# Optimization experiments

Hardware: AMD Instinct MI355X
Metric: run time of the kernel (lower is better)

## Reference

```python
import jax, jax.numpy as jnp
import numpy as np

T, V, D, L, H, F, R = 1024, 17, 1024, 2, 16, 4096, 32
DH = D // H
LORA_SCALE = 2.0  # lora_alpha / r = 64 / 32
MASK_ID = 16
NEG = jnp.float32(-1e9)


def setup_inputs() -> dict:
    key = jax.random.key(0)
    ks = iter(jax.random.split(key, 64))
    def p(shape, std):
        return jax.random.normal(next(ks), shape, jnp.float32) * std
    inp = {
        "packed_context": jax.random.randint(next(ks), (T,), 0, V),
        "cu_seq_lens": jnp.sort(jax.random.randint(next(ks), (5,), 0, T)),
        "max_seq_len": T,
        "row_coords": jax.random.randint(next(ks), (T,), 0, 64),
        "col_coords": jax.random.randint(next(ks), (T,), 0, 64),
        "num_diffusion_steps": 2,
        "E": p((V, D), 0.02),  # embed rows actually used: weight[:vocab_size]
    }
    shapes = {"q": (D, D), "k": (D, D), "v": (D, D), "o": (D, D),
              "g": (D, F), "u": (D, F), "d": (F, D)}
    for nm, (di, do) in shapes.items():
        inp["W" + nm] = p((L, di, do), di ** -0.5)  # frozen NF4 base weight (dequantized)
        inp["A" + nm] = p((L, di, R), di ** -0.5)   # LoRA A
        inp["B" + nm] = p((L, R, do), 0.01)          # LoRA B (nonzero for grad testing)
    inp["ln1"] = jnp.ones((L, D), jnp.float32)
    inp["ln2"] = jnp.ones((L, D), jnp.float32)
    inp["lnf"] = jnp.ones((D,), jnp.float32)
    return inp


def _rms(x, w):
    return x * jax.lax.rsqrt(jnp.mean(x * x, axis=-1, keepdims=True) + 1e-6) * w


def _lora(x, W, A, B):
    # fused base matmul + low-rank LoRA delta
    return x @ W + LORA_SCALE * ((x @ A) @ B)


def _denoise_step(soft, E, Wq, Aq, Bq, Wk, Ak, Bk, Wv, Av, Bv, Wo, Ao, Bo,
                  Wg, Ag, Bg, Wu, Au, Bu, Wd, Ad, Bd, ln1, ln2, lnf, causal_bias):
    # soft-token embedding: [T,V] @ [V,D]
    x = soft @ E
    inv_sqrt_dh = jnp.float32(1.0 / np.sqrt(DH))
    for l in range(L):
        h = _rms(x, ln1[l])
        q = _lora(h, Wq[l], Aq[l], Bq[l]).reshape(T, H, DH)
        k = _lora(h, Wk[l], Ak[l], Bk[l]).reshape(T, H, DH)
        v = _lora(h, Wv[l], Av[l], Bv[l]).reshape(T, H, DH)
        scores = jnp.einsum('qhd,khd->hqk', q, k) * inv_sqrt_dh + causal_bias
        att = jax.nn.softmax(scores, axis=-1)
        ctx = jnp.einsum('hqk,khd->qhd', att, v).reshape(T, D)
        x = x + _lora(ctx, Wo[l], Ao[l], Bo[l])
        h2 = _rms(x, ln2[l])
        ff = jax.nn.silu(_lora(h2, Wg[l], Ag[l], Bg[l])) * _lora(h2, Wu[l], Au[l], Bu[l])
        x = x + _lora(ff, Wd[l], Ad[l], Bd[l])
    logits = _rms(x, lnf) @ E.T  # tied head over the 17-token task vocab
    return jax.nn.softmax(logits, axis=-1)


def reference(packed_context, cu_seq_lens, max_seq_len, row_coords, col_coords,
              num_diffusion_steps, E, Wq, Aq, Bq, Wk, Ak, Bk, Wv, Av, Bv,
              Wo, Ao, Bo, Wg, Ag, Bg, Wu, Au, Bu, Wd, Ad, Bd, ln1, ln2, lnf):
    causal_bias = jnp.where(jnp.tril(jnp.ones((T, T), bool)), jnp.float32(0.0), NEG)
    is_prompt = (packed_context != MASK_ID)[:, None]  # [T,1]
    ctx_onehot = jax.nn.one_hot(packed_context, V, dtype=jnp.float32)
    soft = jnp.zeros((T, V), jnp.float32).at[:, MASK_ID].set(1.0)
    for _ in range(int(num_diffusion_steps)):
        refined = _denoise_step(soft, E, Wq, Aq, Bq, Wk, Ak, Bk, Wv, Av, Bv,
                                Wo, Ao, Bo, Wg, Ag, Bg, Wu, Au, Bu, Wd, Ad, Bd,
                                ln1, ln2, lnf, causal_bias)
        soft = jnp.where(is_prompt, ctx_onehot, refined)
    return jnp.argmax(soft, axis=-1)
```

## Files before the change

### kernel.cpp

```cpp
#include <hip/hip_runtime.h>
#include <hip/hip_bf16.h>

#define T_LEN 1024
#define D_DIM 1024
#define V_DIM 17
#define H_NUM 16
#define DH_DIM 64
#define F_DIM 4096
#define R_LORA 32
#define N_LAYERS 2
#define N_STEPS 2
#define MASK_ID 16
#define LORA_SCALE 2.0f

typedef __attribute__((ext_vector_type(8))) short bfx8;
typedef __attribute__((ext_vector_type(4))) float f32x4;

typedef unsigned short ushort_t;
typedef unsigned int uint_t;

#define AS1 __attribute__((address_space(1)))
#define AS3 __attribute__((address_space(3)))

__device__ __forceinline__ void gload16(const ushort_t* g, ushort_t* l) {
    __builtin_amdgcn_global_load_lds((const AS1 void*)(const void*)g,
                                     (AS3 void*)(void*)l, 16, 0, 0);
}

__device__ __forceinline__ ushort_t f2bf(float v) {
    __hip_bfloat16 h = __float2bfloat16(v);
    return __builtin_bit_cast(unsigned short, h);
}
__device__ __forceinline__ float bf2f(ushort_t u) {
    return __uint_as_float(((uint_t)u) << 16);
}
__device__ __forceinline__ void split4_store(float y0, float y1, float y2, float y3,
                                             ushort_t* __restrict__ hi, ushort_t* __restrict__ lo,
                                             size_t idx) {
    ushort_t h0 = f2bf(y0), h1 = f2bf(y1), h2 = f2bf(y2), h3 = f2bf(y3);
    ushort_t l0 = f2bf(y0 - bf2f(h0));
    ushort_t l1 = f2bf(y1 - bf2f(h1));
    ushort_t l2 = f2bf(y2 - bf2f(h2));
    ushort_t l3 = f2bf(y3 - bf2f(h3));
    uint2 hv, lv;
    hv.x = (uint_t)h0 | ((uint_t)h1 << 16);
    hv.y = (uint_t)h2 | ((uint_t)h3 << 16);
    lv.x = (uint_t)l0 | ((uint_t)l1 << 16);
    lv.y = (uint_t)l2 | ((uint_t)l3 << 16);
    *(uint2*)(hi + idx) = hv;
    *(uint2*)(lo + idx) = lv;
}

__global__ void init_soft_kernel(float* __restrict__ soft) {
    int idx = blockIdx.x * blockDim.x + threadIdx.x;
    if (idx < T_LEN * V_DIM) {
        soft[idx] = ((idx % V_DIM) == MASK_ID) ? 1.0f : 0.0f;
    }
}

__global__ __launch_bounds__(256) void embed_kernel(const float* __restrict__ soft,
                                                    const float* __restrict__ E,
                                                    float* __restrict__ x) {
    int t = blockIdx.x;
    __shared__ float srow[V_DIM];
    if (threadIdx.x < V_DIM) srow[threadIdx.x] = soft[t * V_DIM + threadIdx.x];
    __syncthreads();
    for (int d = threadIdx.x; d < D_DIM; d += 256) {
        float acc = 0.f;
        #pragma unroll
        for (int v = 0; v < V_DIM; v++) acc += srow[v] * E[v * D_DIM + d];
        x[(size_t)t * D_DIM + d] = acc;
    }
}

__global__ __launch_bounds__(256) void fold_kernel(
    const float* __restrict__ W,
    const float* __restrict__ A,
    const float* __restrict__ Bm,
    ushort_t* __restrict__ oHi,
    ushort_t* __restrict__ oLo,
    int K, int N)
{
    const int l = blockIdx.z;
    W   += (size_t)l * K * N;
    A   += (size_t)l * K * R_LORA;
    Bm  += (size_t)l * R_LORA * N;
    oHi += (size_t)l * K * N;
    oLo += (size_t)l * K * N;
    __shared__ uint_t tile[64][65];
    const int tid = threadIdx.x;
    const int n0 = blockIdx.x * 64, k0 = blockIdx.y * 64;
    {
        const int nl = tid & 63, kq = tid >> 6;
        float breg[R_LORA];
        #pragma unroll
        for (int r = 0; r < R_LORA; r++) breg[r] = Bm[(size_t)r * N + n0 + nl];
        for (int i = 0; i < 16; i++) {
            const int kl = kq * 16 + i;
            const size_t kgl = (size_t)(k0 + kl);
            const float4* arow4 = (const float4*)(A + kgl * R_LORA);
            float acc = 0.f;
            #pragma unroll
            for (int r4 = 0; r4 < 8; r4++) {
                float4 a = arow4[r4];
                acc = fmaf(a.x, breg[r4 * 4 + 0], acc);
                acc = fmaf(a.y, breg[r4 * 4 + 1], acc);
                acc = fmaf(a.z, breg[r4 * 4 + 2], acc);
                acc = fmaf(a.w, breg[r4 * 4 + 3], acc);
            }
            float val = W[kgl * N + n0 + nl] + LORA_SCALE * acc;
            ushort_t h = f2bf(val);
            ushort_t l2 = f2bf(val - bf2f(h));
            tile[kl][nl] = ((uint_t)h << 16) | (uint_t)l2;
        }
    }
    __syncthreads();
    {
        const int nl = tid >> 2;
        const int kc0 = (tid & 3) * 16;
        ushort_t hb[16], lb[16];
        #pragma unroll
        for (int i = 0; i < 16; i++) {
            uint_t pk = tile[kc0 + i][nl];
            hb[i] = (ushort_t)(pk >> 16);
            lb[i] = (ushort_t)(pk & 0xffffu);
        }
        size_t idx = (size_t)(n0 + nl) * K + k0 + kc0;
        *(uint4*)(oHi + idx)     = *(uint4*)&hb[0];
        *(uint4*)(oHi + idx + 8) = *(uint4*)&hb[8];
        *(uint4*)(oLo + idx)     = *(uint4*)&lb[0];
        *(uint4*)(oLo + idx + 8) = *(uint4*)&lb[8];
    }
}

__global__ __launch_bounds__(256) void rms_split_kernel(
    const float* __restrict__ x, const float* __restrict__ w,
    ushort_t* __restrict__ hi, ushort_t* __restrict__ lo)
{
    const int t = blockIdx.x, tid = threadIdx.x;
    const float* xr = x + (size_t)t * D_DIM;
    float4 xv = *(const float4*)(xr + tid * 4);
    float ss = xv.x * xv.x + xv.y * xv.y + xv.z * xv.z + xv.w * xv.w;
    __shared__ float red[4];
    const int lane = tid & 63, wv = tid >> 6;
    #pragma unroll
    for (int off = 32; off > 0; off >>= 1) ss += __shfl_xor(ss, off);
    if (lane == 0) red[wv] = ss;
    __syncthreads();
    ss = red[0] + red[1] + red[2] + red[3];
    const float r = 1.0f / sqrtf(ss * (1.0f / D_DIM) + 1e-6f);
    const float4 wv4 = *(const float4*)(w + tid * 4);
    size_t base = (size_t)t * D_DIM + tid * 4;
    split4_store(xv.x * r * wv4.x, xv.y * r * wv4.y, xv.z * r * wv4.z, xv.w * r * wv4.w,
                 hi, lo, base);
}

__global__ __launch_bounds__(256) void add4_rms_split_kernel(
    float* __restrict__ x, const float* __restrict__ p0, const float* __restrict__ p1,
    const float* __restrict__ p2, const float* __restrict__ p3,
    const float* __restrict__ w, ushort_t* __restrict__ hi, ushort_t* __restrict__ lo)
{
    const int t = blockIdx.x, tid = threadIdx.x;
    size_t base = (size_t)t * D_DIM + tid * 4;
    float4 xv = *(const float4*)(x + base);
    float4 a = *(const float4*)(p0 + base);
    float4 b = *(const float4*)(p1 + base);
    float4 c = *(const float4*)(p2 + base);
    float4 d = *(const float4*)(p3 + base);
    xv.x += a.x + b.x + c.x + d.x;
    xv.y += a.y + b.y + c.y + d.y;
    xv.z += a.z + b.z + c.z + d.z;
    xv.w += a.w + b.w + c.w + d.w;
    *(float4*)(x + base) = xv;
    float ss = xv.x * xv.x + xv.y * xv.y + xv.z * xv.z + xv.w * xv.w;
    __shared__ float red[4];
    const int lane = tid & 63, wv = tid >> 6;
    #pragma unroll
    for (int off = 32; off > 0; off >>= 1) ss += __shfl_xor(ss, off);
    if (lane == 0) red[wv] = ss;
    __syncthreads();
    ss = red[0] + red[1] + red[2] + red[3];
    const float r = 1.0f / sqrtf(ss * (1.0f / D_DIM) + 1e-6f);
    const float4 wv4 = *(const float4*)(w + tid * 4);
    split4_store(xv.x * r * wv4.x, xv.y * r * wv4.y, xv.z * r * wv4.z, xv.w * r * wv4.w,
                 hi, lo, base);
}

struct GemmJob {
    const ushort_t* Bh;
    const ushort_t* Bl;
    float* Cf;
    ushort_t* Ch;
    ushort_t* Cl;
    int k0, k1;
};

__global__ __launch_bounds__(256) void gemm128_kernel(
    const ushort_t* __restrict__ Ahi, const ushort_t* __restrict__ Alo,
    int K, int N, GemmJob j0, GemmJob j1, GemmJob j2, GemmJob j3)
{
    GemmJob jb = (blockIdx.z == 0) ? j0 : (blockIdx.z == 1) ? j1 : (blockIdx.z == 2) ? j2 : j3;
    __shared__ ushort_t Ash[128][32];
    __shared__ ushort_t Asl[128][32];
    __shared__ ushort_t Bsh[128][32];
    __shared__ ushort_t Bsl[128][32];

    const int tid = threadIdx.x, lane = tid & 63, w = tid >> 6;
    const int l15 = lane & 15, lg = lane >> 4;
    const int m0 = blockIdx.y * 128, n0 = blockIdx.x * 128;
    const int wm = (w >> 1) * 64, wn = (w & 1) * 64;

    const int r0 = w * 32;
    const int rsub = lane >> 2;
    const int cs = lane & 3;
    const int csl = (cs ^ ((rsub >> 1) & 3)) * 8;
    const int rsl = (lg ^ ((l15 >> 1) & 3)) * 8;

    f32x4 acc[4][4];
    #pragma unroll
    for (int i = 0; i < 4; i++)
        #pragma unroll
        for (int j = 0; j < 4; j++) acc[i][j] = f32x4{0.f, 0.f, 0.f, 0.f};

    const size_t rowA = (size_t)(m0 + r0 + rsub) * K;
    const size_t rowB = (size_t)(n0 + r0 + rsub) * K;
    const size_t rstep = (size_t)16 * K;

    for (int kk = jb.k0; kk < jb.k1; kk += 32) {
        {
            const ushort_t* a0 = Ahi + rowA + kk + csl;
            const ushort_t* a1 = Alo + rowA + kk + csl;
            const ushort_t* b0 = jb.Bh + rowB + kk + csl;
            const ushort_t* b1 = jb.Bl + rowB + kk + csl;
            gload16(a0,         &Ash[r0][0]);
            gload16(a0 + rstep, &Ash[r0 + 16][0]);
            gload16(a1,         &Asl[r0][0]);
            gload16(a1 + rstep, &Asl[r0 + 16][0]);
            gload16(b0,         &Bsh[r0][0]);
            gload16(b0 + rstep, &Bsh[r0 + 16][0]);
            gload16(b1,         &Bsl[r0][0]);
            gload16(b1 + rstep, &Bsl[r0 + 16][0]);
        }
        __syncthreads();
        bfx8 bh[4], bl[4];
        #pragma unroll
        for (int ni = 0; ni < 4; ni++) {
            bh[ni] = *(const bfx8*)&Bsh[wn + ni * 16 + l15][rsl];
            bl[ni] = *(const bfx8*)&Bsl[wn + ni * 16 + l15][rsl];
        }
        #pragma unroll
        for (int mi = 0; mi < 4; mi++) {
            bfx8 ah = *(const bfx8*)&Ash[wm + mi * 16 + l15][rsl];
            bfx8 al = *(const bfx8*)&Asl[wm + mi * 16 + l15][rsl];
            #pragma unroll
            for (int ni = 0; ni < 4; ni++) {
                acc[mi][ni] = __builtin_amdgcn_mfma_f32_16x16x32_bf16(ah, bh[ni], acc[mi][ni], 0, 0, 0);
                acc[mi][ni] = __builtin_amdgcn_mfma_f32_16x16x32_bf16(ah, bl[ni], acc[mi][ni], 0, 0, 0);
                acc[mi][ni] = __builtin_amdgcn_mfma_f32_16x16x32_bf16(al, bh[ni], acc[mi][ni], 0, 0, 0);
            }
        }
        __syncthreads();
    }

    if (jb.Cf) {
        #pragma unroll
        for (int mi = 0; mi < 4; mi++)
            #pragma unroll
            for (int ni = 0; ni < 4; ni++) {
                int col = n0 + wn + ni * 16 + l15;
                #pragma unroll
                for (int i = 0; i < 4; i++) {
                    int row = m0 + wm + mi * 16 + lg * 4 + i;
                    jb.Cf[(size_t)row * N + col] = acc[mi][ni][i];
                }
            }
    } else {
        #pragma unroll
        for (int mi = 0; mi < 4; mi++)
            #pragma unroll
            for (int ni = 0; ni < 4; ni++) {
                int col = n0 + wn + ni * 16 + l15;
                #pragma unroll
                for (int i = 0; i < 4; i++) {
                    int row = m0 + wm + mi * 16 + lg * 4 + i;
                    size_t idx = (size_t)row * N + col;
                    float v = acc[mi][ni][i];
                    ushort_t h = f2bf(v);
                    jb.Ch[idx] = h;
                    jb.Cl[idx] = f2bf(v - bf2f(h));
                }
            }
    }
}

__global__ void add4_kernel(float* __restrict__ x, const float* __restrict__ p0,
                            const float* __restrict__ p1, const float* __restrict__ p2,
                            const float* __restrict__ p3, int n4) {
    int i = blockIdx.x * blockDim.x + threadIdx.x;
    if (i < n4) {
        float4 xv = *(const float4*)(x + (size_t)i * 4);
        float4 a = *(const float4*)(p0 + (size_t)i * 4);
        float4 b = *(const float4*)(p1 + (size_t)i * 4);
        float4 c = *(const float4*)(p2 + (size_t)i * 4);
        float4 d = *(const float4*)(p3 + (size_t)i * 4);
        xv.x += a.x + b.x + c.x + d.x;
        xv.y += a.y + b.y + c.y + d.y;
        xv.z += a.z + b.z + c.z + d.z;
        xv.w += a.w + b.w + c.w + d.w;
        *(float4*)(x + (size_t)i * 4) = xv;
    }
}

#define KS_PAD 72
#define P_PAD 72
__global__ __launch_bounds__(256, 1) void attn_mfma_kernel(
    const ushort_t* __restrict__ qh, const ushort_t* __restrict__ ql,
    const ushort_t* __restrict__ kh, const ushort_t* __restrict__ kl,
    const ushort_t* __restrict__ vh, const ushort_t* __restrict__ vl,
    ushort_t* __restrict__ chi, ushort_t* __restrict__ clo)
{
    __shared__ ushort_t Ksh[64][KS_PAD];
    __shared__ ushort_t Ksl[64][KS_PAD];
    __shared__ ushort_t VTh[64][KS_PAD];
    __shared__ ushort_t VTl[64][KS_PAD];
    __shared__ ushort_t Ph[4][16][P_PAD];
    __shared__ ushort_t Pl[4][16][P_PAD];

    const int qt = blockIdx.x, hh = blockIdx.y;
    const int tid = threadIdx.x, w = tid >> 6, lane = tid & 63;
    const int l15 = lane & 15, lg = lane >> 4;
    const int q0 = qt * 64;
    const int hcol = hh * DH_DIM;

    bfx8 qa_h[2], qa_l[2];
    {
        size_t qrow = (size_t)(q0 + w * 16 + l15) * D_DIM + hcol;
        #pragma unroll
        for (int ks = 0; ks < 2; ks++) {
            qa_h[ks] = *(const bfx8*)(qh + qrow + ks * 32 + lg * 8);
            qa_l[ks] = *(const bfx8*)(ql + qrow + ks * 32 + lg * 8);
        }
    }

    f32x4 o[4];
    #pragma unroll
    for (int ni = 0; ni < 4; ni++) o[ni] = f32x4{0.f, 0.f, 0.f, 0.f};
    float mrun[4], lrun[4];
    #pragma unroll
    for (int i = 0; i < 4; i++) { mrun[i] = -3.0e38f; lrun[i] = 0.f; }

    const int srow = tid >> 2;
    const int sseg = (tid & 3) * 16;
    const int vp = tid & 31;
    const int vd0 = (tid >> 5) * 8;

    for (int kt = 0; kt <= qt; kt++) {
        __syncthreads();
        {
            size_t src = (size_t)(kt * 64 + srow) * D_DIM + hcol + sseg;
            *(uint4*)&Ksh[srow][sseg]     = *(const uint4*)(kh + src);
            *(uint4*)&Ksh[srow][sseg + 8] = *(const uint4*)(kh + src + 8);
            *(uint4*)&Ksl[srow][sseg]     = *(const uint4*)(kl + src);
            *(uint4*)&Ksl[srow][sseg + 8] = *(const uint4*)(kl + src + 8);
        }
        {
            size_t s0 = (size_t)(kt * 64 + 2 * vp) * D_DIM + hcol + vd0;
            uint4 h0 = *(const uint4*)(vh + s0);
            uint4 h1 = *(const uint4*)(vh + s0 + D_DIM);
            uint4 l0 = *(const uint4*)(vl + s0);
            uint4 l1 = *(const uint4*)(vl + s0 + D_DIM);
            const ushort_t* a = (const ushort_t*)&h0;
            const ushort_t* b = (const ushort_t*)&h1;
            const ushort_t* c = (const ushort_t*)&l0;
            const ushort_t* d = (const ushort_t*)&l1;
            #pragma unroll
            for (int j = 0; j < 8; j++) {
                *(uint_t*)&VTh[vd0 + j][2 * vp] = (uint_t)a[j] | ((uint_t)b[j] << 16);
                *(uint_t*)&VTl[vd0 + j][2 * vp] = (uint_t)c[j] | ((uint_t)d[j] << 16);
            }
        }
        __syncthreads();

        f32x4 s[4];
        #pragma unroll
        for (int ni = 0; ni < 4; ni++) s[ni] = f32x4{0.f, 0.f, 0.f, 0.f};
        #pragma unroll
        for (int ks = 0; ks < 2; ks++) {
            #pragma unroll
            for (int ni = 0; ni < 4; ni++) {
                bfx8 bh = *(const bfx8*)&Ksh[ni * 16 + l15][ks * 32 + lg * 8];
                bfx8 bl = *(const bfx8*)&Ksl[ni * 16 + l15][ks * 32 + lg * 8];
                s[ni] = __builtin_amdgcn_mfma_f32_16x16x32_bf16(qa_h[ks], bh, s[ni], 0, 0, 0);
                s[ni] = __builtin_amdgcn_mfma_f32_16x16x32_bf16(qa_h[ks], bl, s[ni], 0, 0, 0);
                s[ni] = __builtin_amdgcn_mfma_f32_16x16x32_bf16(qa_l[ks], bh, s[ni], 0, 0, 0);
            }
        }

        const int kbase = kt * 64;
        float rmax[4];
        #pragma unroll
        for (int i = 0; i < 4; i++) rmax[i] = -3.0e38f;
        #pragma unroll
        for (int ni = 0; ni < 4; ni++) {
            int kc = kbase + ni * 16 + l15;
            #pragma unroll
            for (int i = 0; i < 4; i++) {
                int qrow = q0 + w * 16 + lg * 4 + i;
                float v = s[ni][i] * 0.125f;
                v = (kc <= qrow) ? v : -3.0e38f;
                s[ni][i] = v;
                rmax[i] = fmaxf(rmax[i], v);
            }
        }
        #pragma unroll
        for (int off = 1; off < 16; off <<= 1) {
            #pragma unroll
            for (int i = 0; i < 4; i++) rmax[i] = fmaxf(rmax[i], __shfl_xor(rmax[i], off));
        }
        float psum[4];
        #pragma unroll
        for (int i = 0; i < 4; i++) {
            float nm = fmaxf(mrun[i], rmax[i]);
            float sc = __expf(mrun[i] - nm);
            lrun[i] *= sc;
            #pragma unroll
            for (int ni = 0; ni < 4; ni++) o[ni][i] *= sc;
            mrun[i] = nm;
            psum[i] = 0.f;
        }
        #pragma unroll
        for (int ni = 0; ni < 4; ni++) {
            #pragma unroll
            for (int i = 0; i < 4; i++) {
                float e = __expf(s[ni][i] - mrun[i]);
                s[ni][i] = e;
                psum[i] += e;
            }
        }
        #pragma unroll
        for (int off = 1; off < 16; off <<= 1) {
            #pragma unroll
            for (int i = 0; i < 4; i++) psum[i] += __shfl_xor(psum[i], off);
        }
        #pragma unroll
        for (int i = 0; i < 4; i++) lrun[i] += psum[i];

        #pragma unroll
        for (int ni = 0; ni < 4; ni++) {
            #pragma unroll
            for (int i = 0; i < 4; i++) {
                float e = s[ni][i];
                ushort_t hp = f2bf(e);
                Ph[w][lg * 4 + i][ni * 16 + l15] = hp;
                Pl[w][lg * 4 + i][ni * 16 + l15] = f2bf(e - bf2f(hp));
            }
        }
        #pragma unroll
        for (int ks = 0; ks < 2; ks++) {
            bfx8 ah = *(const bfx8*)&Ph[w][l15][ks * 32 + lg * 8];
            bfx8 al = *(const bfx8*)&Pl[w][l15][ks * 32 + lg * 8];
            #pragma unroll
            for (int ni = 0; ni < 4; ni++) {
                bfx8 bh = *(const bfx8*)&VTh[ni * 16 + l15][ks * 32 + lg * 8];
                bfx8 bl = *(const bfx8*)&VTl[ni * 16 + l15][ks * 32 + lg * 8];
                o[ni] = __builtin_amdgcn_mfma_f32_16x16x32_bf16(ah, bh, o[ni], 0, 0, 0);
                o[ni] = __builtin_amdgcn_mfma_f32_16x16x32_bf16(ah, bl, o[ni], 0, 0, 0);
                o[ni] = __builtin_amdgcn_mfma_f32_16x16x32_bf16(al, bh, o[ni], 0, 0, 0);
            }
        }
    }

    #pragma unroll
    for (int i = 0; i < 4; i++) {
        float inv = 1.0f / lrun[i];
        #pragma unroll
        for (int ni = 0; ni < 4; ni++) o[ni][i] *= inv;
    }
    #pragma unroll
    for (int ni = 0; ni < 4; ni++) {
        int col = hcol + ni * 16 + l15;
        #pragma unroll
        for (int i = 0; i < 4; i++) {
            int row = q0 + w * 16 + lg * 4 + i;
            size_t idx = (size_t)row * D_DIM + col;
            float v = o[ni][i];
            ushort_t hp = f2bf(v);
            chi[idx] = hp;
            clo[idx] = f2bf(v - bf2f(hp));
        }
    }
}

__global__ void silu_split_kernel(const float* __restrict__ g, const float* __restrict__ u,
                                  ushort_t* __restrict__ hi, ushort_t* __restrict__ lo, int n4) {
    int i = blockIdx.x * blockDim.x + threadIdx.x;
    if (i < n4) {
        float4 gv = *(const float4*)(g + (size_t)i * 4);
        float4 uv = *(const float4*)(u + (size_t)i * 4);
        float y0 = gv.x / (1.f + expf(-gv.x)) * uv.x;
        float y1 = gv.y / (1.f + expf(-gv.y)) * uv.y;
        float y2 = gv.z / (1.f + expf(-gv.z)) * uv.z;
        float y3 = gv.w / (1.f + expf(-gv.w)) * uv.w;
        split4_store(y0, y1, y2, y3, hi, lo, (size_t)i * 4);
    }
}

__global__ __launch_bounds__(256) void head_kernel(const float* __restrict__ x,
                                                   const float* __restrict__ lnf,
                                                   const float* __restrict__ E,
                                                   const int* __restrict__ tok,
                                                   float* __restrict__ soft) {
    int t = blockIdx.x;
    int tid = threadIdx.x;
    __shared__ float y[D_DIM];
    __shared__ float red[4];
    __shared__ float logits[V_DIM];
    const float* xr = x + (size_t)t * D_DIM;
    float ss = 0.f;
    for (int d = tid; d < D_DIM; d += 256) { float v = xr[d]; ss += v * v; }
    int lane = tid & 63, wave = tid >> 6;
    for (int off = 32; off > 0; off >>= 1) ss += __shfl_xor(ss, off);
    if (lane == 0) red[wave] = ss;
    __syncthreads();
    ss = red[0] + red[1] + red[2] + red[3];
    float r = 1.0f / sqrtf(ss * (1.0f / D_DIM) + 1e-6f);
    for (int d = tid; d < D_DIM; d += 256) y[d] = xr[d] * r * lnf[d];
    __syncthreads();
    for (int vv = wave; vv < V_DIM; vv += 4) {
        float p = 0.f;
        for (int d = lane; d < D_DIM; d += 64) p += y[d] * E[vv * D_DIM + d];
        for (int off = 32; off > 0; off >>= 1) p += __shfl_xor(p, off);
        if (lane == 0) logits[vv] = p;
    }
    __syncthreads();
    if (tid == 0) {
        int tk = tok[t];
        if (tk != MASK_ID) {
            for (int vv = 0; vv < V_DIM; vv++) soft[t * V_DIM + vv] = (vv == tk) ? 1.f : 0.f;
        } else {
            float mx = -1e30f;
            for (int vv = 0; vv < V_DIM; vv++) mx = fmaxf(mx, logits[vv]);
            float sm = 0.f;
            float e[V_DIM];
            for (int vv = 0; vv < V_DIM; vv++) { e[vv] = expf(logits[vv] - mx); sm += e[vv]; }
            float invs = 1.0f / sm;
            for (int vv = 0; vv < V_DIM; vv++) soft[t * V_DIM + vv] = e[vv] * invs;
        }
    }
}

__global__ void argmax_kernel(const float* __restrict__ soft, int* __restrict__ out) {
    int t = blockIdx.x * blockDim.x + threadIdx.x;
    if (t < T_LEN) {
        const float* s = soft + t * V_DIM;
        int best = 0;
        float bv = s[0];
        #pragma unroll
        for (int vv = 1; vv < V_DIM; vv++) {
            float v = s[vv];
            if (v > bv) { bv = v; best = vv; }
        }
        out[t] = best;
    }
}

__global__ __launch_bounds__(256) void rms_kernel(const float* __restrict__ x,
                                                  const float* __restrict__ w,
                                                  float* __restrict__ out) {
    int t = blockIdx.x;
    const float* xr = x + (size_t)t * D_DIM;
    float ss = 0.f;
    for (int d = threadIdx.x; d < D_DIM; d += 256) { float v = xr[d]; ss += v * v; }
    __shared__ float red[4];
    int lane = threadIdx.x & 63, wave = threadIdx.x >> 6;
    for (int off = 32; off > 0; off >>= 1) ss += __shfl_xor(ss, off);
    if (lane == 0) red[wave] = ss;
    __syncthreads();
    ss = red[0] + red[1] + red[2] + red[3];
    float r = 1.0f / sqrtf(ss * (1.0f / D_DIM) + 1e-6f);
    for (int d = threadIdx.x; d < D_DIM; d += 256) out[(size_t)t * D_DIM + d] = xr[d] * r * w[d];
}

__global__ __launch_bounds__(256) void gemm_kernel(const float* __restrict__ A,
                                                   const float* __restrict__ B,
                                                   float* __restrict__ C,
                                                   int M, int N, int K,
                                                   float alpha, int accumulate) {
    const int BM = 64, BN = 64, BK = 16;
    __shared__ float As[BK][BM];
    __shared__ float Bsh[BK][BN];
    int tid = threadIdx.x;
    int tx = tid % 16, ty = tid / 16;
    int row0 = blockIdx.y * BM, col0 = blockIdx.x * BN;
    float acc[4][4] = {};
    for (int k0 = 0; k0 < K; k0 += BK) {
        #pragma unroll
        for (int i = 0; i < 4; i++) {
            int e = tid * 4 + i;
            int m = e / BK, kk = e % BK;
            int gr = row0 + m, gk = k0 + kk;
            As[kk][m] = (gr < M && gk < K) ? A[(size_t)gr * K + gk] : 0.f;
        }
        #pragma unroll
        for (int i = 0; i < 4; i++) {
            int e = tid * 4 + i;
            int kk = e / BN, n = e % BN;
            int gk = k0 + kk, gc = col0 + n;
            Bsh[kk][n] = (gk < K && gc < N) ? B[(size_t)gk * N + gc] : 0.f;
        }
        __syncthreads();
        #pragma unroll
        for (int kk = 0; kk < BK; kk++) {
            float a[4], b[4];
            #pragma unroll
            for (int i = 0; i < 4; i++) a[i] = As[kk][ty * 4 + i];
            #pragma unroll
            for (int j = 0; j < 4; j++) b[j] = Bsh[kk][tx * 4 + j];
            #pragma unroll
            for (int i = 0; i < 4; i++)
                #pragma unroll
                for (int j = 0; j < 4; j++)
                    acc[i][j] += a[i] * b[j];
        }
        __syncthreads();
    }
    #pragma unroll
    for (int i = 0; i < 4; i++) {
        int r = row0 + ty * 4 + i;
        if (r >= M) continue;
        #pragma unroll
        for (int j = 0; j < 4; j++) {
            int c = col0 + tx * 4 + j;
            if (c >= N) continue;
            size_t idx = (size_t)r * N + c;
            float val = alpha * acc[i][j];
            if (accumulate) val += C[idx];
            C[idx] = val;
        }
    }
}

__global__ __launch_bounds__(256) void attn_kernel(const float* __restrict__ q,
                                                   const float* __restrict__ k,
                                                   const float* __restrict__ v,
                                                   float* __restrict__ ctx) {
    int qi = blockIdx.x;
    int hh = blockIdx.y;
    __shared__ float sc[T_LEN];
    __shared__ float qrow[DH_DIM];
    __shared__ float red[8];
    __shared__ float part[4][DH_DIM];
    int tid = threadIdx.x;
    int lane = tid & 63, wave = tid >> 6;
    const float* qp = q + (size_t)qi * D_DIM + hh * DH_DIM;
    if (tid < DH_DIM) qrow[tid] = qp[tid];
    __syncthreads();
    const float scale = 0.125f;
    for (int j = wave; j <= qi; j += 4) {
        const float* kp = k + (size_t)j * D_DIM + hh * DH_DIM;
        float p = qrow[lane] * kp[lane];
        for (int off = 32; off > 0; off >>= 1) p += __shfl_xor(p, off);
        if (lane == 0) sc[j] = p * scale;
    }
    __syncthreads();
    int n = qi + 1;
    float m = -1e30f;
    for (int j = tid; j < n; j += 256) m = fmaxf(m, sc[j]);
    for (int off = 32; off > 0; off >>= 1) m = fmaxf(m, __shfl_xor(m, off));
    if (lane == 0) red[wave] = m;
    __syncthreads();
    m = fmaxf(fmaxf(red[0], red[1]), fmaxf(red[2], red[3]));
    float s = 0.f;
    for (int j = tid; j < n; j += 256) { float e = expf(sc[j] - m); sc[j] = e; s += e; }
    for (int off = 32; off > 0; off >>= 1) s += __shfl_xor(s, off);
    if (lane == 0) red[4 + wave] = s;
    __syncthreads();
    s = red[4] + red[5] + red[6] + red[7];
    float inv = 1.0f / s;
    float acc = 0.f;
    for (int j = wave; j < n; j += 4) {
        acc += sc[j] * v[(size_t)j * D_DIM + hh * DH_DIM + lane];
    }
    part[wave][lane] = acc;
    __syncthreads();
    if (tid < DH_DIM) {
        float r = (part[0][tid] + part[1][tid] + part[2][tid] + part[3][tid]) * inv;
        ctx[(size_t)qi * D_DIM + hh * DH_DIM + tid] = r;
    }
}

__global__ void silu_mul_kernel(const float* __restrict__ g, const float* __restrict__ u,
                                float* __restrict__ out, int nelem) {
    int i = blockIdx.x * blockDim.x + threadIdx.x;
    if (i < nelem) {
        float gv = g[i];
        float sg = 1.0f / (1.0f + expf(-gv));
        out[i] = gv * sg * u[i];
    }
}

static inline void launch_gemm(const float* A, const float* B, float* C,
                               int M, int N, int K, float alpha, int accumulate,
                               hipStream_t stream) {
    dim3 grid((N + 63) / 64, (M + 63) / 64);
    gemm_kernel<<<grid, 256, 0, stream>>>(A, B, C, M, N, K, alpha, accumulate);
}

extern "C" void kernel_launch(void* const* d_in, const int* in_sizes, int n_in,
                              void* d_out, int out_size, void* d_ws, size_t ws_size,
                              hipStream_t stream) {
    const int* packed = (const int*)d_in[0];
    const float* E  = (const float*)d_in[6];
    const float* Wsrc[7] = {(const float*)d_in[7],  (const float*)d_in[10], (const float*)d_in[13],
                            (const float*)d_in[16], (const float*)d_in[19], (const float*)d_in[22],
                            (const float*)d_in[25]};
    const float* Asrc[7] = {(const float*)d_in[8],  (const float*)d_in[11], (const float*)d_in[14],
                            (const float*)d_in[17], (const float*)d_in[20], (const float*)d_in[23],
                            (const float*)d_in[26]};
    const float* Bsrc[7] = {(const float*)d_in[9],  (const float*)d_in[12], (const float*)d_in[15],
                            (const float*)d_in[18], (const float*)d_in[21], (const float*)d_in[24],
                            (const float*)d_in[27]};
    const float* ln1 = (const float*)d_in[28];
    const float* ln2 = (const float*)d_in[29];
    const float* lnf = (const float*)d_in[30];

    const size_t DD = (size_t)D_DIM * D_DIM;
    const size_t DF = (size_t)D_DIM * F_DIM;
    const size_t wsizes[7] = {DD, DD, DD, DD, DF, DF, DF};
    const int Kdim[7] = {D_DIM, D_DIM, D_DIM, D_DIM, D_DIM, D_DIM, F_DIM};
    const int Ndim[7] = {D_DIM, D_DIM, D_DIM, D_DIM, F_DIM, F_DIM, D_DIM};

    size_t u16_elems = 0;
    for (int p = 0; p < 7; p++) u16_elems += 2ull * N_LAYERS * wsizes[p];
    u16_elems += 2ull * DD;
    u16_elems += 2ull * DD;
    u16_elems += 2ull * DF;
    u16_elems += 6ull * DD;
    size_t f32_elems = (size_t)T_LEN * V_DIM + DD  + 2 * DF ;
    size_t need = u16_elems * 2 + f32_elems * 4 + 256;

    if (ws_size >= need) {
        ushort_t* ub = (ushort_t*)d_ws;
        size_t uo = 0;
        ushort_t *Whi[7], *Wlo[7];
        for (int p = 0; p < 7; p++) {
            Whi[p] = ub + uo; uo += (size_t)N_LAYERS * wsizes[p];
            Wlo[p] = ub + uo; uo += (size_t)N_LAYERS * wsizes[p];
        }
        ushort_t* h_hi = ub + uo; uo += DD;
        ushort_t* h_lo = ub + uo; uo += DD;
        ushort_t* c_hi = ub + uo; uo += DD;
        ushort_t* c_lo = ub + uo; uo += DD;
        ushort_t* f_hi = ub + uo; uo += DF;
        ushort_t* f_lo = ub + uo; uo += DF;
        ushort_t* qbh = ub + uo; uo += DD;
        ushort_t* qbl = ub + uo; uo += DD;
        ushort_t* kbh = ub + uo; uo += DD;
        ushort_t* kbl = ub + uo; uo += DD;
        ushort_t* vbh = ub + uo; uo += DD;
        ushort_t* vbl = ub + uo; uo += DD;
        float* fb = (float*)(ub + uo);
        size_t fo = 0;
        float* soft = fb + fo; fo += (size_t)T_LEN * V_DIM;
        float* x    = fb + fo; fo += DD;
        float* gbuf = fb + fo; fo += DF;
        float* ubuf = fb + fo; fo += DF;
        float* p0 = gbuf;
        float* p1 = gbuf + DD;
        float* p2 = gbuf + 2 * DD;
        float* p3 = gbuf + 3 * DD;

        for (int p = 0; p < 7; p++) {
            dim3 grid(Ndim[p] / 64, Kdim[p] / 64, N_LAYERS);
            fold_kernel<<<grid, 256, 0, stream>>>(Wsrc[p], Asrc[p], Bsrc[p],
                                                  Whi[p], Wlo[p], Kdim[p], Ndim[p]);
        }

        init_soft_kernel<<<(T_LEN * V_DIM + 255) / 256, 256, 0, stream>>>(soft);

        const int n4 = (int)(DD / 4);
        for (int step = 0; step < N_STEPS; step++) {
            embed_kernel<<<T_LEN, 256, 0, stream>>>(soft, E, x);
            rms_split_kernel<<<T_LEN, 256, 0, stream>>>(x, ln1, h_hi, h_lo);
            for (int l = 0; l < N_LAYERS; l++) {
                {
                    GemmJob jq = {Whi[0] + l * DD, Wlo[0] + l * DD, nullptr, qbh, qbl, 0, D_DIM};
                    GemmJob jk = {Whi[1] + l * DD, Wlo[1] + l * DD, nullptr, kbh, kbl, 0, D_DIM};
                    GemmJob jv = {Whi[2] + l * DD, Wlo[2] + l * DD, nullptr, vbh, vbl, 0, D_DIM};
                    gemm128_kernel<<<dim3(8, 8, 3), 256, 0, stream>>>(
                        h_hi, h_lo, D_DIM, D_DIM, jq, jk, jv, jq);
                }
                attn_mfma_kernel<<<dim3(T_LEN / 64, H_NUM), 256, 0, stream>>>(
                    qbh, qbl, kbh, kbl, vbh, vbl, c_hi, c_lo);
                {
                    const ushort_t* bh = Whi[3] + l * DD;
                    const ushort_t* bl = Wlo[3] + l * DD;
                    GemmJob ja = {bh, bl, p0, nullptr, nullptr, 0, 256};
                    GemmJob jb = {bh, bl, p1, nullptr, nullptr, 256, 512};
                    GemmJob jc = {bh, bl, p2, nullptr, nullptr, 512, 768};
                    GemmJob jd = {bh, bl, p3, nullptr, nullptr, 768, 1024};
                    gemm128_kernel<<<dim3(8, 8, 4), 256, 0, stream>>>(
                        c_hi, c_lo, D_DIM, D_DIM, ja, jb, jc, jd);
                    add4_rms_split_kernel<<<T_LEN, 256, 0, stream>>>(
                        x, p0, p1, p2, p3, ln2 + (size_t)l * D_DIM, h_hi, h_lo);
                }
                {
                    GemmJob jg = {Whi[4] + l * DF, Wlo[4] + l * DF, gbuf, nullptr, nullptr, 0, D_DIM};
                    GemmJob ju = {Whi[5] + l * DF, Wlo[5] + l * DF, ubuf, nullptr, nullptr, 0, D_DIM};
                    gemm128_kernel<<<dim3(32, 8, 2), 256, 0, stream>>>(
                        h_hi, h_lo, D_DIM, F_DIM, jg, ju, jg, jg);
                }
                silu_split_kernel<<<(T_LEN * F_DIM / 4 + 255) / 256, 256, 0, stream>>>(
                    gbuf, ubuf, f_hi, f_lo, T_LEN * F_DIM / 4);
                {
                    const ushort_t* bh = Whi[6] + l * DF;
                    const ushort_t* bl = Wlo[6] + l * DF;
                    GemmJob ja = {bh, bl, p0, nullptr, nullptr, 0, 1024};
                    GemmJob jb = {bh, bl, p1, nullptr, nullptr, 1024, 2048};
                    GemmJob jc = {bh, bl, p2, nullptr, nullptr, 2048, 3072};
                    GemmJob jd = {bh, bl, p3, nullptr, nullptr, 3072, 4096};
                    gemm128_kernel<<<dim3(8, 8, 4), 256, 0, stream>>>(
                        f_hi, f_lo, F_DIM, D_DIM, ja, jb, jc, jd);
                    if (l + 1 < N_LAYERS) {
                        add4_rms_split_kernel<<<T_LEN, 256, 0, stream>>>(
                            x, p0, p1, p2, p3, ln1 + (size_t)(l + 1) * D_DIM, h_hi, h_lo);
                    } else {
                        add4_kernel<<<(n4 + 255) / 256, 256, 0, stream>>>(x, p0, p1, p2, p3, n4);
                    }
                }
            }
            head_kernel<<<T_LEN, 256, 0, stream>>>(x, lnf, E, packed, soft);
        }
        argmax_kernel<<<(T_LEN + 255) / 256, 256, 0, stream>>>(soft, (int*)d_out);
        return;
    }

    float* ws = (float*)d_ws;
    size_t off = 0;
    float* soft = ws + off; off += (size_t)T_LEN * V_DIM;
    float* x    = ws + off; off += (size_t)T_LEN * D_DIM;
    float* h    = ws + off; off += (size_t)T_LEN * D_DIM;
    float* qb   = ws + off; off += (size_t)T_LEN * D_DIM;
    float* kb   = ws + off; off += (size_t)T_LEN * D_DIM;
    float* vb   = ws + off; off += (size_t)T_LEN * D_DIM;
    float* cb   = ws + off; off += (size_t)T_LEN * D_DIM;
    float* gb   = ws + off; off += (size_t)T_LEN * F_DIM;
    float* ubf  = ws + off; off += (size_t)T_LEN * F_DIM;
    float* tmp  = ws + off; off += (size_t)T_LEN * R_LORA;

    init_soft_kernel<<<(T_LEN * V_DIM + 255) / 256, 256, 0, stream>>>(soft);
    for (int step = 0; step < N_STEPS; step++) {
        embed_kernel<<<T_LEN, 256, 0, stream>>>(soft, E, x);
        for (int l = 0; l < N_LAYERS; l++) {
            const float* ln1_l = ln1 + (size_t)l * D_DIM;
            const float* ln2_l = ln2 + (size_t)l * D_DIM;
            rms_kernel<<<T_LEN, 256, 0, stream>>>(x, ln1_l, h);
            launch_gemm(h, Asrc[0] + (size_t)l * D_DIM * R_LORA, tmp, T_LEN, R_LORA, D_DIM, 1.0f, 0, stream);
            launch_gemm(h, Wsrc[0] + (size_t)l * DD, qb, T_LEN, D_DIM, D_DIM, 1.0f, 0, stream);
            launch_gemm(tmp, Bsrc[0] + (size_t)l * R_LORA * D_DIM, qb, T_LEN, D_DIM, R_LORA, LORA_SCALE, 1, stream);
            launch_gemm(h, Asrc[1] + (size_t)l * D_DIM * R_LORA, tmp, T_LEN, R_LORA, D_DIM, 1.0f, 0, stream);
            launch_gemm(h, Wsrc[1] + (size_t)l * DD, kb, T_LEN, D_DIM, D_DIM, 1.0f, 0, stream);
            launch_gemm(tmp, Bsrc[1] + (size_t)l * R_LORA * D_DIM, kb, T_LEN, D_DIM, R_LORA, LORA_SCALE, 1, stream);
            launch_gemm(h, Asrc[2] + (size_t)l * D_DIM * R_LORA, tmp, T_LEN, R_LORA, D_DIM, 1.0f, 0, stream);
            launch_gemm(h, Wsrc[2] + (size_t)l * DD, vb, T_LEN, D_DIM, D_DIM, 1.0f, 0, stream);
            launch_gemm(tmp, Bsrc[2] + (size_t)l * R_LORA * D_DIM, vb, T_LEN, D_DIM, R_LORA, LORA_SCALE, 1, stream);
            attn_kernel<<<dim3(T_LEN, H_NUM), 256, 0, stream>>>(qb, kb, vb, cb);
            launch_gemm(cb, Asrc[3] + (size_t)l * D_DIM * R_LORA, tmp, T_LEN, R_LORA, D_DIM, 1.0f, 0, stream);
            launch_gemm(cb, Wsrc[3] + (size_t)l * DD, x, T_LEN, D_DIM, D_DIM, 1.0f, 1, stream);
            launch_gemm(tmp, Bsrc[3] + (size_t)l * R_LORA * D_DIM, x, T_LEN, D_DIM, R_LORA, LORA_SCALE, 1, stream);
            rms_kernel<<<T_LEN, 256, 0, stream>>>(x, ln2_l, h);
            launch_gemm(h, Asrc[4] + (size_t)l * D_DIM * R_LORA, tmp, T_LEN, R_LORA, D_DIM, 1.0f, 0, stream);
            launch_gemm(h, Wsrc[4] + (size_t)l * DF, gb, T_LEN, F_DIM, D_DIM, 1.0f, 0, stream);
            launch_gemm(tmp, Bsrc[4] + (size_t)l * R_LORA * F_DIM, gb, T_LEN, F_DIM, R_LORA, LORA_SCALE, 1, stream);
            launch_gemm(h, Asrc[5] + (size_t)l * D_DIM * R_LORA, tmp, T_LEN, R_LORA, D_DIM, 1.0f, 0, stream);
            launch_gemm(h, Wsrc[5] + (size_t)l * DF, ubf, T_LEN, F_DIM, D_DIM, 1.0f, 0, stream);
            launch_gemm(tmp, Bsrc[5] + (size_t)l * R_LORA * F_DIM, ubf, T_LEN, F_DIM, R_LORA, LORA_SCALE, 1, stream);
            silu_mul_kernel<<<(T_LEN * F_DIM + 255) / 256, 256, 0, stream>>>(gb, ubf, gb, T_LEN * F_DIM);
            launch_gemm(gb, Asrc[6] + (size_t)l * F_DIM * R_LORA, tmp, T_LEN, R_LORA, F_DIM, 1.0f, 0, stream);
            launch_gemm(gb, Wsrc[6] + (size_t)l * DF, x, T_LEN, D_DIM, F_DIM, 1.0f, 1, stream);
            launch_gemm(tmp, Bsrc[6] + (size_t)l * R_LORA * D_DIM, x, T_LEN, D_DIM, R_LORA, LORA_SCALE, 1, stream);
        }
        head_kernel<<<T_LEN, 256, 0, stream>>>(x, lnf, E, packed, soft);
    }
    argmax_kernel<<<(T_LEN + 255) / 256, 256, 0, stream>>>(soft, (int*)d_out);
}
```

Before: 1.229 ms.

## Increase split-K parallelism across GEMMs and fuse embed with RMS split

The QKV GEMM becomes a 6-way split-K launch and the O-proj and down-proj GEMMs become 8-way split-K launches, raising block count to fill more CUs. A new reduction kernel sums the QKV partials and does the hi/lo split, and the add kernels now sum eight partials. The embedding is fused with the first RMS-norm split, and the LoRA fold kernel stages A in shared memory and preloads W. In exchange there is more partial-buffer traffic and extra reduction passes, plus one additional kernel launch for QKV.

```diff
diff --git a/kernel.cpp b/kernel.cpp
--- a/kernel.cpp
+++ b/kernel.cpp
@@ -58,19 +58,40 @@
     }
 }
 
-__global__ __launch_bounds__(256) void embed_kernel(const float* __restrict__ soft,
-                                                    const float* __restrict__ E,
-                                                    float* __restrict__ x) {
-    int t = blockIdx.x;
+__global__ __launch_bounds__(256) void embed_rms_split_kernel(
+    const float* __restrict__ soft, const float* __restrict__ E,
+    const float* __restrict__ w, float* __restrict__ x,
+    ushort_t* __restrict__ hi, ushort_t* __restrict__ lo)
+{
+    const int t = blockIdx.x, tid = threadIdx.x;
     __shared__ float srow[V_DIM];
-    if (threadIdx.x < V_DIM) srow[threadIdx.x] = soft[t * V_DIM + threadIdx.x];
-    __syncthreads();
-    for (int d = threadIdx.x; d < D_DIM; d += 256) {
-        float acc = 0.f;
-        #pragma unroll
-        for (int v = 0; v < V_DIM; v++) acc += srow[v] * E[v * D_DIM + d];
-        x[(size_t)t * D_DIM + d] = acc;
-    }
+    __shared__ float red[4];
+    if (tid < V_DIM) srow[tid] = soft[t * V_DIM + tid];
+    __syncthreads();
+    const int d0 = tid * 4;
+    float4 acc = {0.f, 0.f, 0.f, 0.f};
+    #pragma unroll
+    for (int v = 0; v < V_DIM; v++) {
+        float s = srow[v];
+        float4 e = *(const float4*)(E + (size_t)v * D_DIM + d0);
+        acc.x = fmaf(s, e.x, acc.x);
+        acc.y = fmaf(s, e.y, acc.y);
+        acc.z = fmaf(s, e.z, acc.z);
+        acc.w = fmaf(s, e.w, acc.w);
+    }
+    size_t base = (size_t)t * D_DIM + d0;
+    *(float4*)(x + base) = acc;
+    float ss = acc.x * acc.x + acc.y * acc.y + acc.z * acc.z + acc.w * acc.w;
+    const int lane = tid & 63, wv = tid >> 6;
+    #pragma unroll
+    for (int off = 32; off > 0; off >>= 1) ss += __shfl_xor(ss, off);
+    if (lane == 0) red[wv] = ss;
+    __syncthreads();
+    ss = red[0] + red[1] + red[2] + red[3];
+    const float r = 1.0f / sqrtf(ss * (1.0f / D_DIM) + 1e-6f);
+    const float4 wv4 = *(const float4*)(w + d0);
+    split4_store(acc.x * r * wv4.x, acc.y * r * wv4.y, acc.z * r * wv4.z, acc.w * r * wv4.w,
+                 hi, lo, base);
 }
 
 __global__ __launch_bounds__(256) void fold_kernel(
@@ -87,103 +108,57 @@
     Bm  += (size_t)l * R_LORA * N;
     oHi += (size_t)l * K * N;
     oLo += (size_t)l * K * N;
+    __shared__ float Als[64][R_LORA + 1];
     __shared__ uint_t tile[64][65];
     const int tid = threadIdx.x;
     const int n0 = blockIdx.x * 64, k0 = blockIdx.y * 64;
+
     {
-        const int nl = tid & 63, kq = tid >> 6;
-        float breg[R_LORA];
-        #pragma unroll
-        for (int r = 0; r < R_LORA; r++) breg[r] = Bm[(size_t)r * N + n0 + nl];
-        for (int i = 0; i < 16; i++) {
-            const int kl = kq * 16 + i;
-            const size_t kgl = (size_t)(k0 + kl);
-            const float4* arow4 = (const float4*)(A + kgl * R_LORA);
-            float acc = 0.f;
-            #pragma unroll
-            for (int r4 = 0; r4 < 8; r4++) {
-                float4 a = arow4[r4];
-                acc = fmaf(a.x, breg[r4 * 4 + 0], acc);
-                acc = fmaf(a.y, breg[r4 * 4 + 1], acc);
-                acc = fmaf(a.z, breg[r4 * 4 + 2], acc);
-                acc = fmaf(a.w, breg[r4 * 4 + 3], acc);
-            }
-            float val = W[kgl * N + n0 + nl] + LORA_SCALE * acc;
-            ushort_t h = f2bf(val);
-            ushort_t l2 = f2bf(val - bf2f(h));
-            tile[kl][nl] = ((uint_t)h << 16) | (uint_t)l2;
-        }
+        const int row = tid >> 2, c0 = (tid & 3) * 8;
+        const float* src = A + (size_t)(k0 + row) * R_LORA + c0;
+        float4 a0 = *(const float4*)(src);
+        float4 a1 = *(const float4*)(src + 4);
+        Als[row][c0 + 0] = a0.x; Als[row][c0 + 1] = a0.y;
+        Als[row][c0 + 2] = a0.z; Als[row][c0 + 3] = a0.w;
+        Als[row][c0 + 4] = a1.x; Als[row][c0 + 5] = a1.y;
+        Als[row][c0 + 6] = a1.z; Als[row][c0 + 7] = a1.w;
+    }
+    const int nl = tid & 63, kq = tid >> 6;
+    float wreg[16];
+    #pragma unroll
+    for (int i = 0; i < 16; i++)
+        wreg[i] = W[(size_t)(k0 + kq * 16 + i) * N + n0 + nl];
+    float breg[R_LORA];
+    #pragma unroll
+    for (int r = 0; r < R_LORA; r++) breg[r] = Bm[(size_t)r * N + n0 + nl];
+    __syncthreads();
+    #pragma unroll
+    for (int i = 0; i < 16; i++) {
+        const int kl = kq * 16 + i;
+        float acc = 0.f;
+        #pragma unroll
+        for (int r = 0; r < R_LORA; r++) acc = fmaf(Als[kl][r], breg[r], acc);
+        float val = wreg[i] + LORA_SCALE * acc;
+        ushort_t h = f2bf(val);
+        tile[kl][nl] = ((uint_t)h << 16) | (uint_t)f2bf(val - bf2f(h));
     }
     __syncthreads();
     {
-        const int nl = tid >> 2;
+        const int nl2 = tid >> 2;
         const int kc0 = (tid & 3) * 16;
         ushort_t hb[16], lb[16];
         #pragma unroll
         for (int i = 0; i < 16; i++) {
-            uint_t pk = tile[kc0 + i][nl];
+            uint_t pk = tile[kc0 + i][nl2];
             hb[i] = (ushort_t)(pk >> 16);
             lb[i] = (ushort_t)(pk & 0xffffu);
         }
-        size_t idx = (size_t)(n0 + nl) * K + k0 + kc0;
+        size_t idx = (size_t)(n0 + nl2) * K + k0 + kc0;
         *(uint4*)(oHi + idx)     = *(uint4*)&hb[0];
         *(uint4*)(oHi + idx + 8) = *(uint4*)&hb[8];
         *(uint4*)(oLo + idx)     = *(uint4*)&lb[0];
         *(uint4*)(oLo + idx + 8) = *(uint4*)&lb[8];
     }
-}
-
-__global__ __launch_bounds__(256) void rms_split_kernel(
-    const float* __restrict__ x, const float* __restrict__ w,
-    ushort_t* __restrict__ hi, ushort_t* __restrict__ lo)
-{
-    const int t = blockIdx.x, tid = threadIdx.x;
-    const float* xr = x + (size_t)t * D_DIM;
-    float4 xv = *(const float4*)(xr + tid * 4);
-    float ss = xv.x * xv.x + xv.y * xv.y + xv.z * xv.z + xv.w * xv.w;
-    __shared__ float red[4];
-    const int lane = tid & 63, wv = tid >> 6;
-    #pragma unroll
-    for (int off = 32; off > 0; off >>= 1) ss += __shfl_xor(ss, off);
-    if (lane == 0) red[wv] = ss;
-    __syncthreads();
-    ss = red[0] + red[1] + red[2] + red[3];
-    const float r = 1.0f / sqrtf(ss * (1.0f / D_DIM) + 1e-6f);
-    const float4 wv4 = *(const float4*)(w + tid * 4);
-    size_t base = (size_t)t * D_DIM + tid * 4;
-    split4_store(xv.x * r * wv4.x, xv.y * r * wv4.y, xv.z * r * wv4.z, xv.w * r * wv4.w,
-                 hi, lo, base);
-}
-
-__global__ __launch_bounds__(256) void add4_rms_split_kernel(
-    float* __restrict__ x, const float* __restrict__ p0, const float* __restrict__ p1,
-    const float* __restrict__ p2, const float* __restrict__ p3,
-    const float* __restrict__ w, ushort_t* __restrict__ hi, ushort_t* __restrict__ lo)
-{
-    const int t = blockIdx.x, tid = threadIdx.x;
-    size_t base = (size_t)t * D_DIM + tid * 4;
-    float4 xv = *(const float4*)(x + base);
-    float4 a = *(const float4*)(p0 + base);
-    float4 b = *(const float4*)(p1 + base);
-    float4 c = *(const float4*)(p2 + base);
-    float4 d = *(const float4*)(p3 + base);
-    xv.x += a.x + b.x + c.x + d.x;
-    xv.y += a.y + b.y + c.y + d.y;
-    xv.z += a.z + b.z + c.z + d.z;
-    xv.w += a.w + b.w + c.w + d.w;
-    *(float4*)(x + base) = xv;
-    float ss = xv.x * xv.x + xv.y * xv.y + xv.z * xv.z + xv.w * xv.w;
-    __shared__ float red[4];
-    const int lane = tid & 63, wv = tid >> 6;
-    #pragma unroll
-    for (int off = 32; off > 0; off >>= 1) ss += __shfl_xor(ss, off);
-    if (lane == 0) red[wv] = ss;
-    __syncthreads();
-    ss = red[0] + red[1] + red[2] + red[3];
-    const float r = 1.0f / sqrtf(ss * (1.0f / D_DIM) + 1e-6f);
-    const float4 wv4 = *(const float4*)(w + tid * 4);
-    split4_store(xv.x * r * wv4.x, xv.y * r * wv4.y, xv.z * r * wv4.z, xv.w * r * wv4.w,
-                 hi, lo, base);
 }
 
 struct GemmJob {
@@ -197,9 +172,18 @@
 
 __global__ __launch_bounds__(256) void gemm128_kernel(
     const ushort_t* __restrict__ Ahi, const ushort_t* __restrict__ Alo,
-    int K, int N, GemmJob j0, GemmJob j1, GemmJob j2, GemmJob j3)
+    int K, int N,
+    GemmJob j0, GemmJob j1, GemmJob j2, GemmJob j3,
+    GemmJob j4, GemmJob j5, GemmJob j6, GemmJob j7)
 {
-    GemmJob jb = (blockIdx.z == 0) ? j0 : (blockIdx.z == 1) ? j1 : (blockIdx.z == 2) ? j2 : j3;
+    GemmJob jb;
+    {
+        const int z = blockIdx.z;
+        if      (z == 0) jb = j0; else if (z == 1) jb = j1;
+        else if (z == 2) jb = j2; else if (z == 3) jb = j3;
+        else if (z == 4) jb = j4; else if (z == 5) jb = j5;
+        else if (z == 6) jb = j6; else jb = j7;
+    }
     __shared__ ushort_t Ash[128][32];
     __shared__ ushort_t Asl[128][32];
     __shared__ ushort_t Bsh[128][32];
@@ -293,22 +277,67 @@
     }
 }
 
-__global__ void add4_kernel(float* __restrict__ x, const float* __restrict__ p0,
-                            const float* __restrict__ p1, const float* __restrict__ p2,
-                            const float* __restrict__ p3, int n4) {
+__global__ __launch_bounds__(256) void qkv2_split_kernel(
+    const float* __restrict__ pb,
+    ushort_t* __restrict__ qbh, ushort_t* __restrict__ qbl,
+    ushort_t* __restrict__ kbh, ushort_t* __restrict__ kbl,
+    ushort_t* __restrict__ vbh, ushort_t* __restrict__ vbl)
+{
+    const size_t DD1 = (size_t)T_LEN * D_DIM;
+    size_t e = ((size_t)blockIdx.x * 256 + threadIdx.x) * 4;
+    float4 a, b;
+    a = *(const float4*)(pb + e);
+    b = *(const float4*)(pb + DD1 + e);
+    split4_store(a.x + b.x, a.y + b.y, a.z + b.z, a.w + b.w, qbh, qbl, e);
+    a = *(const float4*)(pb + 2 * DD1 + e);
+    b = *(const float4*)(pb + 3 * DD1 + e);
+    split4_store(a.x + b.x, a.y + b.y, a.z + b.z, a.w + b.w, kbh, kbl, e);
+    a = *(const float4*)(pb + 4 * DD1 + e);
+    b = *(const float4*)(pb + 5 * DD1 + e);
+    split4_store(a.x + b.x, a.y + b.y, a.z + b.z, a.w + b.w, vbh, vbl, e);
+}
+
+__global__ void add8_kernel(float* __restrict__ x, const float* __restrict__ pb, int n4) {
     int i = blockIdx.x * blockDim.x + threadIdx.x;
     if (i < n4) {
-        float4 xv = *(const float4*)(x + (size_t)i * 4);
-        float4 a = *(const float4*)(p0 + (size_t)i * 4);
-        float4 b = *(const float4*)(p1 + (size_t)i * 4);
-        float4 c = *(const float4*)(p2 + (size_t)i * 4);
-        float4 d = *(const float4*)(p3 + (size_t)i * 4);
-        xv.x += a.x + b.x + c.x + d.x;
-        xv.y += a.y + b.y + c.y + d.y;
-        xv.z += a.z + b.z + c.z + d.z;
-        xv.w += a.w + b.w + c.w + d.w;
-        *(float4*)(x + (size_t)i * 4) = xv;
-    }
+        const size_t DD1 = (size_t)T_LEN * D_DIM;
+        size_t e = (size_t)i * 4;
+        float4 xv = *(const float4*)(x + e);
+        #pragma unroll
+        for (int j = 0; j < 8; j++) {
+            float4 p = *(const float4*)(pb + j * DD1 + e);
+            xv.x += p.x; xv.y += p.y; xv.z += p.z; xv.w += p.w;
+        }
+        *(float4*)(x + e) = xv;
+    }
+}
+
+__global__ __launch_bounds__(256) void add8_rms_split_kernel(
+    float* __restrict__ x, const float* __restrict__ pb,
+    const float* __restrict__ w, ushort_t* __restrict__ hi, ushort_t* __restrict__ lo)
+{
+    const int t = blockIdx.x, tid = threadIdx.x;
+    const size_t DD1 = (size_t)T_LEN * D_DIM;
+    size_t base = (size_t)t * D_DIM + tid * 4;
+    float4 xv = *(const float4*)(x + base);
+    #pragma unroll
+    for (int j = 0; j < 8; j++) {
+        float4 p = *(const float4*)(pb + j * DD1 + base);
+        xv.x += p.x; xv.y += p.y; xv.z += p.z; xv.w += p.w;
+    }
+    *(float4*)(x + base) = xv;
+    float ss = xv.x * xv.x + xv.y * xv.y + xv.z * xv.z + xv.w * xv.w;
+    __shared__ float red[4];
+    const int lane = tid & 63, wv = tid >> 6;
+    #pragma unroll
+    for (int off = 32; off > 0; off >>= 1) ss += __shfl_xor(ss, off);
+    if (lane == 0) red[wv] = ss;
+    __syncthreads();
+    ss = red[0] + red[1] + red[2] + red[3];
+    const float r = 1.0f / sqrtf(ss * (1.0f / D_DIM) + 1e-6f);
+    const float4 wv4 = *(const float4*)(w + tid * 4);
+    split4_store(xv.x * r * wv4.x, xv.y * r * wv4.y, xv.z * r * wv4.z, xv.w * r * wv4.w,
+                 hi, lo, base);
 }
 
 #define KS_PAD 72
@@ -579,6 +608,21 @@
     ss = red[0] + red[1] + red[2] + red[3];
     float r = 1.0f / sqrtf(ss * (1.0f / D_DIM) + 1e-6f);
     for (int d = threadIdx.x; d < D_DIM; d += 256) out[(size_t)t * D_DIM + d] = xr[d] * r * w[d];
+}
+
+__global__ __launch_bounds__(256) void embed_kernel(const float* __restrict__ soft,
+                                                    const float* __restrict__ E,
+                                                    float* __restrict__ x) {
+    int t = blockIdx.x;
+    __shared__ float srow[V_DIM];
+    if (threadIdx.x < V_DIM) srow[threadIdx.x] = soft[t * V_DIM + threadIdx.x];
+    __syncthreads();
+    for (int d = threadIdx.x; d < D_DIM; d += 256) {
+        float acc = 0.f;
+        #pragma unroll
+        for (int v = 0; v < V_DIM; v++) acc += srow[v] * E[v * D_DIM + d];
+        x[(size_t)t * D_DIM + d] = acc;
+    }
 }
 
 __global__ __launch_bounds__(256) void gemm_kernel(const float* __restrict__ A,
@@ -765,10 +809,7 @@
         float* x    = fb + fo; fo += DD;
         float* gbuf = fb + fo; fo += DF;
         float* ubuf = fb + fo; fo += DF;
-        float* p0 = gbuf;
-        float* p1 = gbuf + DD;
-        float* p2 = gbuf + 2 * DD;
-        float* p3 = gbuf + 3 * DD;
+        float* pbase = gbuf;
 
         for (int p = 0; p < 7; p++) {
             dim3 grid(Ndim[p] / 64, Kdim[p] / 64, N_LAYERS);
@@ -780,52 +821,54 @@
 
         const int n4 = (int)(DD / 4);
         for (int step = 0; step < N_STEPS; step++) {
-            embed_kernel<<<T_LEN, 256, 0, stream>>>(soft, E, x);
-            rms_split_kernel<<<T_LEN, 256, 0, stream>>>(x, ln1, h_hi, h_lo);
+            embed_rms_split_kernel<<<T_LEN, 256, 0, stream>>>(soft, E, ln1, x, h_hi, h_lo);
             for (int l = 0; l < N_LAYERS; l++) {
                 {
-                    GemmJob jq = {Whi[0] + l * DD, Wlo[0] + l * DD, nullptr, qbh, qbl, 0, D_DIM};
-                    GemmJob jk = {Whi[1] + l * DD, Wlo[1] + l * DD, nullptr, kbh, kbl, 0, D_DIM};
-                    GemmJob jv = {Whi[2] + l * DD, Wlo[2] + l * DD, nullptr, vbh, vbl, 0, D_DIM};
-                    gemm128_kernel<<<dim3(8, 8, 3), 256, 0, stream>>>(
-                        h_hi, h_lo, D_DIM, D_DIM, jq, jk, jv, jq);
+                    GemmJob jq0 = {Whi[0] + l * DD, Wlo[0] + l * DD, pbase + 0 * DD, nullptr, nullptr, 0, 512};
+                    GemmJob jq1 = {Whi[0] + l * DD, Wlo[0] + l * DD, pbase + 1 * DD, nullptr, nullptr, 512, 1024};
+                    GemmJob jk0 = {Whi[1] + l * DD, Wlo[1] + l * DD, pbase + 2 * DD, nullptr, nullptr, 0, 512};
+                    GemmJob jk1 = {Whi[1] + l * DD, Wlo[1] + l * DD, pbase + 3 * DD, nullptr, nullptr, 512, 1024};
+                    GemmJob jv0 = {Whi[2] + l * DD, Wlo[2] + l * DD, pbase + 4 * DD, nullptr, nullptr, 0, 512};
+                    GemmJob jv1 = {Whi[2] + l * DD, Wlo[2] + l * DD, pbase + 5 * DD, nullptr, nullptr, 512, 1024};
+                    gemm128_kernel<<<dim3(8, 8, 6), 256, 0, stream>>>(
+                        h_hi, h_lo, D_DIM, D_DIM, jq0, jq1, jk0, jk1, jv0, jv1, jq0, jq0);
+                    qkv2_split_kernel<<<(int)(DD / 4 / 256), 256, 0, stream>>>(
+                        pbase, qbh, qbl, kbh, kbl, vbh, vbl);
                 }
                 attn_mfma_kernel<<<dim3(T_LEN / 64, H_NUM), 256, 0, stream>>>(
                     qbh, qbl, kbh, kbl, vbh, vbl, c_hi, c_lo);
                 {
                     const ushort_t* bh = Whi[3] + l * DD;
                     const ushort_t* bl = Wlo[3] + l * DD;
-                    GemmJob ja = {bh, bl, p0, nullptr, nullptr, 0, 256};
-                    GemmJob jb = {bh, bl, p1, nullptr, nullptr, 256, 512};
-                    GemmJob jc = {bh, bl, p2, nullptr, nullptr, 512, 768};
-                    GemmJob jd = {bh, bl, p3, nullptr, nullptr, 768, 1024};
-                    gemm128_kernel<<<dim3(8, 8, 4), 256, 0, stream>>>(
-                        c_hi, c_lo, D_DIM, D_DIM, ja, jb, jc, jd);
-                    add4_rms_split_kernel<<<T_LEN, 256, 0, stream>>>(
-                        x, p0, p1, p2, p3, ln2 + (size_t)l * D_DIM, h_hi, h_lo);
+                    GemmJob j[8];
+                    for (int i = 0; i < 8; i++)
+                        j[i] = {bh, bl, pbase + i * DD, nullptr, nullptr, i * 128, (i + 1) * 128};
+                    gemm128_kernel<<<dim3(8, 8, 8), 256, 0, stream>>>(
+                        c_hi, c_lo, D_DIM, D_DIM, j[0], j[1], j[2], j[3], j[4], j[5], j[6], j[7]);
+                    add8_rms_split_kernel<<<T_LEN, 256, 0, stream>>>(
+                        x, pbase, ln2 + (size_t)l * D_DIM, h_hi, h_lo);
                 }
                 {
                     GemmJob jg = {Whi[4] + l * DF, Wlo[4] + l * DF, gbuf, nullptr, nullptr, 0, D_DIM};
                     GemmJob ju = {Whi[5] + l * DF, Wlo[5] + l * DF, ubuf, nullptr, nullptr, 0, D_DIM};
                     gemm128_kernel<<<dim3(32, 8, 2), 256, 0, stream>>>(
-                        h_hi, h_lo, D_DIM, F_DIM, jg, ju, jg, jg);
+                        h_hi, h_lo, D_DIM, F_DIM, jg, ju, jg, jg, jg, jg, jg, jg);
                 }
                 silu_split_kernel<<<(T_LEN * F_DIM / 4 + 255) / 256, 256, 0, stream>>>(
                     gbuf, ubuf, f_hi, f_lo, T_LEN * F_DIM / 4);
                 {
                     const ushort_t* bh = Whi[6] + l * DF;
                     const ushort_t* bl = Wlo[6] + l * DF;
-                    GemmJob ja = {bh, bl, p0, nullptr, nullptr, 0, 1024};
-                    GemmJob jb = {bh, bl, p1, nullptr, nullptr, 1024, 2048};
-                    GemmJob jc = {bh, bl, p2, nullptr, nullptr, 2048, 3072};
-                    GemmJob jd = {bh, bl, p3, nullptr, nullptr, 3072, 4096};
-                    gemm128_kernel<<<dim3(8, 8, 4), 256, 0, stream>>>(
-                        f_hi, f_lo, F_DIM, D_DIM, ja, jb, jc, jd);
+                    GemmJob j[8];
+                    for (int i = 0; i < 8; i++)
+                        j[i] = {bh, bl, pbase + i * DD, nullptr, nullptr, i * 512, (i + 1) * 512};
+                    gemm128_kernel<<<dim3(8, 8, 8), 256, 0, stream>>>(
+                        f_hi, f_lo, F_DIM, D_DIM, j[0], j[1], j[2], j[3], j[4], j[5], j[6], j[7]);
                     if (l + 1 < N_LAYERS) {
-                        add4_rms_split_kernel<<<T_LEN, 256, 0, stream>>>(
-                            x, p0, p1, p2, p3, ln1 + (size_t)(l + 1) * D_DIM, h_hi, h_lo);
+                        add8_rms_split_kernel<<<T_LEN, 256, 0, stream>>>(
+                            x, pbase, ln1 + (size_t)(l + 1) * D_DIM, h_hi, h_lo);
                     } else {
-                        add4_kernel<<<(n4 + 255) / 256, 256, 0, stream>>>(x, p0, p1, p2, p3, n4);
+                        add8_kernel<<<(n4 + 255) / 256, 256, 0, stream>>>(x, pbase, n4);
                     }
                 }
             }
```

Result: faster. 1.083 ms (-11.9%).
